# Performance work log

Measured on AMD Instinct MI355X. Metric: run time of the kernel, lower is better.

## Reference

```python
import jax, jax.numpy as jnp
import numpy as np

N_ROWS = 8192
EMBED_DIM = 256


def setup_inputs() -> dict:
    key = jax.random.key(0)
    k1, k2, k3, k4, k5 = jax.random.split(key, 5)
    M = jax.random.normal(k1, (N_ROWS, EMBED_DIM), dtype=jnp.float32)
    N = jax.random.normal(k2, (N_ROWS, EMBED_DIM), dtype=jnp.float32)
    # gate_w: nn.Linear(embed_dim, 1) -> weight [1, d], bias [1]; gate_b extra scalar param [1]
    Wg = jax.random.normal(k3, (1, EMBED_DIM), dtype=jnp.float32) * 0.06
    bg = jax.random.normal(k4, (1,), dtype=jnp.float32) * 0.1
    gate_b = jax.random.normal(k5, (1,), dtype=jnp.float32) * 0.1
    return {"M": M, "N": N, "Wg": Wg, "bg": bg, "gate_b": gate_b, "iseval": 0}


def reference(M, N, Wg, bg, gate_b, iseval):
    # mt: [n, n] cross-similarity scores
    mt = jnp.matmul(N, M.T)
    if not iseval:
        # training branch: zero out the diagonal (mt - diag(diag(mt)))
        n = mt.shape[0]
        idx = jnp.arange(n)
        mt = mt.at[idx, idx].set(0.0)
    else:
        # eval branch: zero out the first row
        mt = mt.at[0].set(0.0)
    attn_weight = jax.nn.softmax(mt, axis=-1)          # [n, n]
    out_attn = jnp.matmul(attn_weight, M)              # [n, d]
    gate = jax.nn.sigmoid(jnp.matmul(out_attn, Wg.T) + bg + gate_b)  # [n, 1]
    boosted = out_attn * gate + N * (1.0 - gate)       # [n, d]
    return boosted[:, None, None, :]                   # [n, 1, 1, d]
```

## Files before the change

### kernel.cpp

```cpp
#include <hip/hip_runtime.h>


constexpr int EMBED = 256;
constexpr int BQ = 64;
constexpr int BJ = 32;
constexpr int NT = 256;

constexpr int MH0  = 0;
constexpr int MH1  = 16384;
constexpr int MT0  = 32768;
constexpr int MT1  = 49152;
constexpr int SS_O = 65536;
constexpr int PH_O = 74752;
constexpr int MS_O = 79872;
constexpr int LS_O = 80128;
constexpr int AS_O = 80384;
constexpr int LDS_TOTAL = 80640;

typedef _Float16 half8 __attribute__((ext_vector_type(8)));
typedef float f32x4 __attribute__((ext_vector_type(4)));
typedef short short8v __attribute__((ext_vector_type(8)));

static __device__ __forceinline__ f32x4 mfma16(half8 a, half8 b, f32x4 c) {
    return __builtin_amdgcn_mfma_f32_16x16x32_f16(a, b, c, 0, 0, 0);
}
static __device__ __forceinline__ void gld_lds16(const void* g, void* l) {
    __builtin_amdgcn_global_load_lds((const __attribute__((address_space(1))) unsigned int*)g,
                                     (__attribute__((address_space(3))) unsigned int*)l, 16, 0, 0);
}
static __device__ __forceinline__ short f2h(float x) {
    return (short)__builtin_bit_cast(unsigned short, (_Float16)x);
}

__global__ void prep(const float* __restrict__ M,
                     short* __restrict__ MhG, short* __restrict__ MtG) {
    __shared__ float L[32 * 260];
    const int blk = blockIdx.x;
    const int t = threadIdx.x;
    {
        const float* src = M + (size_t)(blk * 32 + (t >> 3)) * EMBED + (t & 7) * 32;
        float* lr = L + (t >> 3) * 260 + (t & 7) * 32;
        #pragma unroll
        for (int i = 0; i < 8; ++i)
            *(float4*)(lr + 4 * i) = *(const float4*)(src + 4 * i);
    }
    __syncthreads();
    {
        const int j = t >> 3, key = j & 7;
        short* dst = MhG + (size_t)(blk * 32 + j) * 256;
        #pragma unroll
        for (int cc = 0; cc < 4; ++cc) {
            int c = (t & 7) * 4 + cc;
            short8v v;
            #pragma unroll
            for (int e = 0; e < 8; ++e) v[e] = f2h(L[j * 260 + c * 8 + e]);
            *(short8v*)(dst + (c ^ key) * 8) = v;
        }
    }
    {
        const int P = t >> 1, hv = t & 1;
        short* dst = MtG + (size_t)blk * 8192 + P * 64;
        #pragma unroll
        for (int pp = 0; pp < 4; ++pp) {
            int p = hv * 4 + pp;
            int c = p ^ (P & 7);
            int d = 2 * P + (c >> 2), jc = c & 3;
            short8v v;
            #pragma unroll
            for (int e = 0; e < 8; ++e) v[e] = f2h(L[(jc * 8 + e) * 260 + d]);
            *(short8v*)(dst + p * 8) = v;
        }
    }
}

__launch_bounds__(NT, 2)
__global__ void attn_split4(const short* __restrict__ MhG, const short* __restrict__ MtG,
                            const float* __restrict__ Ng, const int* __restrict__ iseval_p,
                            float* __restrict__ O0out, short* __restrict__ Ofp,
                            float* __restrict__ MLm, float* __restrict__ MLl, int n)
{
    __shared__ __align__(16) char smem[LDS_TOTAL];
    float* SS = (float*)(smem + SS_O);
    float* MS = (float*)(smem + MS_O);
    float* LS = (float*)(smem + LS_O);
    float* AS = (float*)(smem + AS_O);

    const int t = threadIdx.x, lane = t & 63, wave = t >> 6;
    const int quad = lane >> 4, mn = lane & 15;
    const int qb = blockIdx.x & 127, s = blockIdx.x >> 7;
    const int q0 = qb * BQ;
    const int jbase = s * (n >> 2);
    const int ntiles = (n >> 2) / BJ;
    const int iseval = *iseval_p;
    const int qp = wave >> 1;
    const int jt = wave & 1;
    const int dh = wave & 1;
    const int sq = t >> 2, sh = t & 3;

    if (t < BQ) { MS[t] = -1e30f; LS[t] = 0.f; }

    half8 Qf[2][8];
    #pragma unroll
    for (int qi = 0; qi < 2; ++qi) {
        const float* np = Ng + (size_t)(q0 + (2 * qp + qi) * 16 + mn) * EMBED;
        #pragma unroll
        for (int ks = 0; ks < 8; ++ks) {
            const float* p = np + ks * 32 + quad * 8;
            float4 a = *(const float4*)p, b = *(const float4*)(p + 4);
            half8 h;
            h[0]=(_Float16)a.x; h[1]=(_Float16)a.y; h[2]=(_Float16)a.z; h[3]=(_Float16)a.w;
            h[4]=(_Float16)b.x; h[5]=(_Float16)b.y; h[6]=(_Float16)b.z; h[7]=(_Float16)b.w;
            Qf[qi][ks] = h;
        }
    }

    {
        const char* mh = (const char*)MhG + (size_t)jbase * 512;
        const char* mt = (const char*)MtG + (size_t)jbase * 512;
        #pragma unroll
        for (int i = 0; i < 4; ++i) {
            int cb = wave * 4 + i;
            gld_lds16(mh + cb * 1024 + lane * 16, smem + MH0 + cb * 1024);
            gld_lds16(mt + cb * 1024 + lane * 16, smem + MT0 + cb * 1024);
        }
    }

    f32x4 O[2][8];
    #pragma unroll
    for (int qi = 0; qi < 2; ++qi)
        #pragma unroll
        for (int dt = 0; dt < 8; ++dt) O[qi][dt] = (f32x4){0.f, 0.f, 0.f, 0.f};

    __syncthreads();

    const int brow = jt * 16 + mn;
    const int bkey = brow & 7;

    for (int tile = 0; tile < ntiles; ++tile) {
        const int cur = tile & 1;
        const char* mhc = smem + (cur ? MH1 : MH0);
        char*       mhn = smem + (cur ? MH0 : MH1);
        const char* mtc = smem + (cur ? MT1 : MT0);
        char*       mtn = smem + (cur ? MT0 : MT1);
        const int j0g = jbase + tile * BJ;
        const bool hn = (tile + 1) < ntiles;

        if (hn) {
            const char* mh = (const char*)MhG + (size_t)(j0g + BJ) * 512;
            #pragma unroll
            for (int i = 0; i < 4; ++i) {
                int cb = wave * 4 + i;
                gld_lds16(mh + cb * 1024 + lane * 16, mhn + cb * 1024);
            }
        }

        {
            f32x4 a0 = (f32x4){0.f,0.f,0.f,0.f}, a1 = (f32x4){0.f,0.f,0.f,0.f};
            #pragma unroll
            for (int ks = 0; ks < 8; ++ks) {
                half8 bf = *(const half8*)(mhc + brow * 512 + (((4 * ks + quad) ^ bkey) << 4));
                a0 = mfma16(Qf[0][ks], bf, a0);
                a1 = mfma16(Qf[1][ks], bf, a1);
            }
            #pragma unroll
            for (int r = 0; r < 4; ++r) {
                SS[((2 * qp) * 16 + quad * 4 + r) * 36 + jt * 16 + mn]     = a0[r];
                SS[((2 * qp + 1) * 16 + quad * 4 + r) * 36 + jt * 16 + mn] = a1[r];
            }
        }
        __syncthreads();

        if (hn) {
            const char* mt = (const char*)MtG + (size_t)(j0g + BJ) * 512;
            #pragma unroll
            for (int i = 0; i < 4; ++i) {
                int cb = wave * 4 + i;
                gld_lds16(mt + cb * 1024 + lane * 16, mtn + cb * 1024);
            }
        }

        {
            float4 sa = *(const float4*)(SS + sq * 36 + 8 * sh);
            float4 sb = *(const float4*)(SS + sq * 36 + 8 * sh + 4);
            float sv[8] = {sa.x, sa.y, sa.z, sa.w, sb.x, sb.y, sb.z, sb.w};
            const int qg = q0 + sq;
            if (iseval) {
                if (qg == 0) {
                    #pragma unroll
                    for (int i = 0; i < 8; ++i) sv[i] = 0.f;
                }
            } else {
                int dj = qg - j0g - 8 * sh;
                #pragma unroll
                for (int i = 0; i < 8; ++i) if (dj == i) sv[i] = 0.f;
            }
            float mx = sv[0];
            #pragma unroll
            for (int i = 1; i < 8; ++i) mx = fmaxf(mx, sv[i]);
            mx = fmaxf(mx, __shfl_xor(mx, 1));
            mx = fmaxf(mx, __shfl_xor(mx, 2));
            float m_old = MS[sq];
            float m_new = fmaxf(m_old, mx);
            float alpha = __expf(m_old - m_new);
            float p[8], ps = 0.f;
            #pragma unroll
            for (int i = 0; i < 8; ++i) { p[i] = __expf(sv[i] - m_new); ps += p[i]; }
            ps += __shfl_xor(ps, 1);
            ps += __shfl_xor(ps, 2);
            if (sh == 0) {
                MS[sq] = m_new;
                AS[sq] = alpha;
                LS[sq] = LS[sq] * alpha + ps;
            }
            half8 ph;
            #pragma unroll
            for (int i = 0; i < 8; ++i) ph[i] = (_Float16)p[i];
            *(half8*)(smem + PH_O + sq * 80 + sh * 16) = ph;
        }
        __syncthreads();

        {
            float aq[2][4];
            #pragma unroll
            for (int qi = 0; qi < 2; ++qi)
                #pragma unroll
                for (int r = 0; r < 4; ++r)
                    aq[qi][r] = AS[(2 * qp + qi) * 16 + quad * 4 + r];
            half8 pa[2];
            #pragma unroll
            for (int qi = 0; qi < 2; ++qi)
                pa[qi] = *(const half8*)(smem + PH_O + ((2 * qp + qi) * 16 + mn) * 80 + quad * 16);
            #pragma unroll
            for (int dt = 0; dt < 8; ++dt) {
                int d = dh * 128 + dt * 16 + mn;
                int P2 = d >> 1;
                int p = ((d & 1) * 4 + quad) ^ (P2 & 7);
                half8 bf = *(const half8*)(mtc + P2 * 128 + p * 16);
                #pragma unroll
                for (int qi = 0; qi < 2; ++qi) {
                    f32x4 o = O[qi][dt];
                    o[0] *= aq[qi][0]; o[1] *= aq[qi][1]; o[2] *= aq[qi][2]; o[3] *= aq[qi][3];
                    O[qi][dt] = mfma16(pa[qi], bf, o);
                }
            }
        }
    }

    if (s == 0) {
        #pragma unroll
        for (int qi = 0; qi < 2; ++qi) {
            int qtb = q0 + (2 * qp + qi) * 16;
            #pragma unroll
            for (int dt = 0; dt < 8; ++dt) {
                int col = dh * 128 + dt * 16 + mn;
                #pragma unroll
                for (int r = 0; r < 4; ++r)
                    O0out[(size_t)(qtb + quad * 4 + r) * EMBED + col] = O[qi][dt][r];
            }
        }
    } else {
        short* dst = Ofp + (size_t)(s - 1) * n * EMBED;
        #pragma unroll
        for (int qi = 0; qi < 2; ++qi) {
            int qtb = q0 + (2 * qp + qi) * 16;
            #pragma unroll
            for (int dt = 0; dt < 8; ++dt) {
                int col = dh * 128 + dt * 16 + mn;
                #pragma unroll
                for (int r = 0; r < 4; ++r)
                    dst[(size_t)(qtb + quad * 4 + r) * EMBED + col] = f2h(O[qi][dt][r]);
            }
        }
    }
    if (t < BQ) {
        MLm[s * n + q0 + t] = MS[t];
        MLl[s * n + q0 + t] = LS[t];
    }
}

__global__ void combine4(const float* __restrict__ O0, const short* __restrict__ Ofp,
                         const float* __restrict__ MLm, const float* __restrict__ MLl,
                         const float* __restrict__ Ng, const float* __restrict__ Wg,
                         const float* __restrict__ bg, const float* __restrict__ gb,
                         float* __restrict__ out, int n)
{
    const int t = threadIdx.x;
    const int row = blockIdx.x * 16 + (t >> 4);
    const int c = t & 15;
    float ms[4], ls[4];
    #pragma unroll
    for (int s = 0; s < 4; ++s) { ms[s] = MLm[s * n + row]; ls[s] = MLl[s * n + row]; }
    float m = fmaxf(fmaxf(ms[0], ms[1]), fmaxf(ms[2], ms[3]));
    float w[4], lsum = 0.f;
    #pragma unroll
    for (int s = 0; s < 4; ++s) { w[s] = __expf(ms[s] - m); lsum += w[s] * ls[s]; }
    float linv = 1.f / lsum;

    float acc[16];
    {
        const float4* o0 = (const float4*)(O0 + (size_t)row * EMBED + c * 16);
        #pragma unroll
        for (int i = 0; i < 4; ++i) {
            float4 v = o0[i];
            acc[4*i+0] = w[0] * v.x; acc[4*i+1] = w[0] * v.y;
            acc[4*i+2] = w[0] * v.z; acc[4*i+3] = w[0] * v.w;
        }
    }
    #pragma unroll
    for (int s = 1; s < 4; ++s) {
        const short* op = Ofp + (size_t)(s - 1) * n * EMBED + (size_t)row * EMBED + c * 16;
        half8 a = *(const half8*)op, b = *(const half8*)(op + 8);
        #pragma unroll
        for (int i = 0; i < 8; ++i) {
            acc[i]     += w[s] * (float)a[i];
            acc[8 + i] += w[s] * (float)b[i];
        }
    }
    float dot = 0.f;
    #pragma unroll
    for (int i = 0; i < 16; ++i) { acc[i] *= linv; dot += acc[i] * Wg[c * 16 + i]; }
    dot += __shfl_xor(dot, 1);
    dot += __shfl_xor(dot, 2);
    dot += __shfl_xor(dot, 4);
    dot += __shfl_xor(dot, 8);
    float g = 1.f / (1.f + __expf(-(dot + bg[0] + gb[0])));
    const float4* n4 = (const float4*)(Ng + (size_t)row * EMBED + c * 16);
    float4* o4 = (float4*)(out + (size_t)row * EMBED + c * 16);
    #pragma unroll
    for (int i = 0; i < 4; ++i) {
        float4 nn = n4[i];
        float4 res;
        res.x = acc[4*i+0] * g + nn.x * (1.f - g);
        res.y = acc[4*i+1] * g + nn.y * (1.f - g);
        res.z = acc[4*i+2] * g + nn.z * (1.f - g);
        res.w = acc[4*i+3] * g + nn.w * (1.f - g);
        o4[i] = res;
    }
}

extern "C" void kernel_launch(void* const* d_in, const int* in_sizes, int n_in,
                              void* d_out, int out_size, void* d_ws, size_t ws_size,
                              hipStream_t stream) {
    const float* M      = (const float*)d_in[0];
    const float* N      = (const float*)d_in[1];
    const float* Wgp    = (const float*)d_in[2];
    const float* bgp    = (const float*)d_in[3];
    const float* gbp    = (const float*)d_in[4];
    const int*   iseval = (const int*)d_in[5];
    float* out = (float*)d_out;

    int n = in_sizes[0] / EMBED;
    short* MhG = (short*)d_ws;
    short* MtG = MhG + (size_t)n * EMBED;
    short* Ofp = MtG + (size_t)n * EMBED;
    float* MLm = (float*)(Ofp + (size_t)3 * n * EMBED);
    float* MLl = MLm + 4 * n;

    hipLaunchKernelGGL(prep, dim3(n / 32), dim3(256), 0, stream, M, MhG, MtG);
    hipLaunchKernelGGL(attn_split4, dim3((n / BQ) * 4), dim3(NT), 0, stream,
                       MhG, MtG, N, iseval, out, Ofp, MLm, MLl, n);
    hipLaunchKernelGGL(combine4, dim3(n / 16), dim3(256), 0, stream,
                       out, Ofp, MLm, MLl, N, Wgp, bgp, gbp, out, n);
}
```

Baseline: 217.7 us.

## Load K/V fragments straight from global into registers, split QK by K-halves

```diff
diff --git a/kernel.cpp b/kernel.cpp
--- a/kernel.cpp
+++ b/kernel.cpp
@@ -6,16 +6,12 @@
 constexpr int BJ = 32;
 constexpr int NT = 256;
 
-constexpr int MH0  = 0;
-constexpr int MH1  = 16384;
-constexpr int MT0  = 32768;
-constexpr int MT1  = 49152;
-constexpr int SS_O = 65536;
-constexpr int PH_O = 74752;
-constexpr int MS_O = 79872;
-constexpr int LS_O = 80128;
-constexpr int AS_O = 80384;
-constexpr int LDS_TOTAL = 80640;
+constexpr int SS_OFF = 0;
+constexpr int PH_OFF = 18432;
+constexpr int MS_OFF = 23552;
+constexpr int LS_OFF = 23808;
+constexpr int AS_OFF = 24064;
+constexpr int LDS_SZ = 24320;
 
 typedef _Float16 half8 __attribute__((ext_vector_type(8)));
 typedef float f32x4 __attribute__((ext_vector_type(4)));
@@ -24,165 +20,149 @@
 static __device__ __forceinline__ f32x4 mfma16(half8 a, half8 b, f32x4 c) {
     return __builtin_amdgcn_mfma_f32_16x16x32_f16(a, b, c, 0, 0, 0);
 }
-static __device__ __forceinline__ void gld_lds16(const void* g, void* l) {
-    __builtin_amdgcn_global_load_lds((const __attribute__((address_space(1))) unsigned int*)g,
-                                     (__attribute__((address_space(3))) unsigned int*)l, 16, 0, 0);
-}
 static __device__ __forceinline__ short f2h(float x) {
     return (short)__builtin_bit_cast(unsigned short, (_Float16)x);
 }
 
 __global__ void prep(const float* __restrict__ M,
                      short* __restrict__ MhG, short* __restrict__ MtG) {
-    __shared__ float L[32 * 260];
-    const int blk = blockIdx.x;
+    __shared__ float L[16 * 260];
+    const int r0 = blockIdx.x * 16;
     const int t = threadIdx.x;
+    const int pj = t >> 4, pc = (t & 15) * 16;
     {
-        const float* src = M + (size_t)(blk * 32 + (t >> 3)) * EMBED + (t & 7) * 32;
-        float* lr = L + (t >> 3) * 260 + (t & 7) * 32;
-        #pragma unroll
-        for (int i = 0; i < 8; ++i)
-            *(float4*)(lr + 4 * i) = *(const float4*)(src + 4 * i);
+        const float* src = M + (size_t)(r0 + pj) * EMBED + pc;
+        float4 v[4];
+        #pragma unroll
+        for (int i = 0; i < 4; ++i) v[i] = ((const float4*)src)[i];
+        short* hd = MhG + (size_t)(r0 + pj) * EMBED + pc;
+        #pragma unroll
+        for (int i = 0; i < 2; ++i) {
+            float4 a = v[2 * i], b = v[2 * i + 1];
+            short8v h;
+            h[0]=f2h(a.x); h[1]=f2h(a.y); h[2]=f2h(a.z); h[3]=f2h(a.w);
+            h[4]=f2h(b.x); h[5]=f2h(b.y); h[6]=f2h(b.z); h[7]=f2h(b.w);
+            *(short8v*)(hd + 8 * i) = h;
+        }
+        #pragma unroll
+        for (int i = 0; i < 4; ++i)
+            *(float4*)(L + pj * 260 + pc + 4 * i) = v[i];
     }
     __syncthreads();
     {
-        const int j = t >> 3, key = j & 7;
-        short* dst = MhG + (size_t)(blk * 32 + j) * 256;
-        #pragma unroll
-        for (int cc = 0; cc < 4; ++cc) {
-            int c = (t & 7) * 4 + cc;
-            short8v v;
-            #pragma unroll
-            for (int e = 0; e < 8; ++e) v[e] = f2h(L[j * 260 + c * 8 + e]);
-            *(short8v*)(dst + (c ^ key) * 8) = v;
-        }
-    }
-    {
-        const int P = t >> 1, hv = t & 1;
-        short* dst = MtG + (size_t)blk * 8192 + P * 64;
-        #pragma unroll
-        for (int pp = 0; pp < 4; ++pp) {
-            int p = hv * 4 + pp;
-            int c = p ^ (P & 7);
-            int d = 2 * P + (c >> 2), jc = c & 3;
-            short8v v;
-            #pragma unroll
-            for (int e = 0; e < 8; ++e) v[e] = f2h(L[(jc * 8 + e) * 260 + d]);
-            *(short8v*)(dst + p * 8) = v;
+        const int d = t;
+        const int tile = r0 >> 5, jh = (r0 >> 4) & 1;
+        short* dst = MtG + (size_t)tile * (BJ * EMBED) + d * BJ + jh * 16;
+        #pragma unroll
+        for (int g2 = 0; g2 < 2; ++g2) {
+            short8v w;
+            #pragma unroll
+            for (int e = 0; e < 8; ++e) w[e] = f2h(L[(g2 * 8 + e) * 260 + d]);
+            *(short8v*)(dst + g2 * 8) = w;
         }
     }
 }
 
 __launch_bounds__(NT, 2)
-__global__ void attn_split4(const short* __restrict__ MhG, const short* __restrict__ MtG,
-                            const float* __restrict__ Ng, const int* __restrict__ iseval_p,
-                            float* __restrict__ O0out, short* __restrict__ Ofp,
-                            float* __restrict__ MLm, float* __restrict__ MLl, int n)
+__global__ void attn(const short* __restrict__ MhG, const short* __restrict__ MtG,
+                     const float* __restrict__ Ng, const int* __restrict__ iseval_p,
+                     float* __restrict__ O0out, short* __restrict__ Ofp,
+                     float* __restrict__ MLm, float* __restrict__ MLl, int n)
 {
-    __shared__ __align__(16) char smem[LDS_TOTAL];
-    float* SS = (float*)(smem + SS_O);
-    float* MS = (float*)(smem + MS_O);
-    float* LS = (float*)(smem + LS_O);
-    float* AS = (float*)(smem + AS_O);
+    __shared__ __align__(16) char smem[LDS_SZ];
+    float* MS = (float*)(smem + MS_OFF);
+    float* LS = (float*)(smem + LS_OFF);
+    float* AS = (float*)(smem + AS_OFF);
 
     const int t = threadIdx.x, lane = t & 63, wave = t >> 6;
     const int quad = lane >> 4, mn = lane & 15;
-    const int qb = blockIdx.x & 127, s = blockIdx.x >> 7;
+    const int bid = blockIdx.x;
+    const int s  = (bid & 7) >> 1;
+    const int qb = ((bid >> 3) << 1) | (bid & 1);
     const int q0 = qb * BQ;
     const int jbase = s * (n >> 2);
+    const int jb32 = jbase / BJ;
     const int ntiles = (n >> 2) / BJ;
     const int iseval = *iseval_p;
-    const int qp = wave >> 1;
-    const int jt = wave & 1;
-    const int dh = wave & 1;
+    const int jt = wave & 1, kh = wave >> 1;
+    const int dq = wave;
     const int sq = t >> 2, sh = t & 3;
 
     if (t < BQ) { MS[t] = -1e30f; LS[t] = 0.f; }
 
-    half8 Qf[2][8];
-    #pragma unroll
-    for (int qi = 0; qi < 2; ++qi) {
-        const float* np = Ng + (size_t)(q0 + (2 * qp + qi) * 16 + mn) * EMBED;
-        #pragma unroll
-        for (int ks = 0; ks < 8; ++ks) {
-            const float* p = np + ks * 32 + quad * 8;
+    half8 Qf[4][4];
+    #pragma unroll
+    for (int qi = 0; qi < 4; ++qi) {
+        const float* np = Ng + (size_t)(q0 + qi * 16 + mn) * EMBED;
+        #pragma unroll
+        for (int kk = 0; kk < 4; ++kk) {
+            const float* p = np + (kh * 4 + kk) * 32 + quad * 8;
             float4 a = *(const float4*)p, b = *(const float4*)(p + 4);
             half8 h;
             h[0]=(_Float16)a.x; h[1]=(_Float16)a.y; h[2]=(_Float16)a.z; h[3]=(_Float16)a.w;
             h[4]=(_Float16)b.x; h[5]=(_Float16)b.y; h[6]=(_Float16)b.z; h[7]=(_Float16)b.w;
-            Qf[qi][ks] = h;
-        }
-    }
-
-    {
-        const char* mh = (const char*)MhG + (size_t)jbase * 512;
-        const char* mt = (const char*)MtG + (size_t)jbase * 512;
-        #pragma unroll
-        for (int i = 0; i < 4; ++i) {
-            int cb = wave * 4 + i;
-            gld_lds16(mh + cb * 1024 + lane * 16, smem + MH0 + cb * 1024);
-            gld_lds16(mt + cb * 1024 + lane * 16, smem + MT0 + cb * 1024);
-        }
-    }
-
-    f32x4 O[2][8];
-    #pragma unroll
-    for (int qi = 0; qi < 2; ++qi)
-        #pragma unroll
-        for (int dt = 0; dt < 8; ++dt) O[qi][dt] = (f32x4){0.f, 0.f, 0.f, 0.f};
+            Qf[qi][kk] = h;
+        }
+    }
+
+    f32x4 O[4][4];
+    #pragma unroll
+    for (int qi = 0; qi < 4; ++qi)
+        #pragma unroll
+        for (int dt = 0; dt < 4; ++dt) O[qi][dt] = (f32x4){0.f, 0.f, 0.f, 0.f};
+
+    const short* mhb0 = MhG + (size_t)(jbase + jt * 16 + mn) * EMBED + kh * 128 + quad * 8;
+    half8 Bc[4], Bn[4], Mtf[4];
+    #pragma unroll
+    for (int kk = 0; kk < 4; ++kk) Bc[kk] = *(const half8*)(mhb0 + kk * 32);
 
     __syncthreads();
 
-    const int brow = jt * 16 + mn;
-    const int bkey = brow & 7;
-
     for (int tile = 0; tile < ntiles; ++tile) {
-        const int cur = tile & 1;
-        const char* mhc = smem + (cur ? MH1 : MH0);
-        char*       mhn = smem + (cur ? MH0 : MH1);
-        const char* mtc = smem + (cur ? MT1 : MT0);
-        char*       mtn = smem + (cur ? MT0 : MT1);
         const int j0g = jbase + tile * BJ;
-        const bool hn = (tile + 1) < ntiles;
-
-        if (hn) {
-            const char* mh = (const char*)MhG + (size_t)(j0g + BJ) * 512;
-            #pragma unroll
-            for (int i = 0; i < 4; ++i) {
-                int cb = wave * 4 + i;
-                gld_lds16(mh + cb * 1024 + lane * 16, mhn + cb * 1024);
-            }
-        }
 
         {
-            f32x4 a0 = (f32x4){0.f,0.f,0.f,0.f}, a1 = (f32x4){0.f,0.f,0.f,0.f};
-            #pragma unroll
-            for (int ks = 0; ks < 8; ++ks) {
-                half8 bf = *(const half8*)(mhc + brow * 512 + (((4 * ks + quad) ^ bkey) << 4));
-                a0 = mfma16(Qf[0][ks], bf, a0);
-                a1 = mfma16(Qf[1][ks], bf, a1);
-            }
+            f32x4 a0 = (f32x4){0,0,0,0}, a1 = (f32x4){0,0,0,0};
+            f32x4 a2 = (f32x4){0,0,0,0}, a3 = (f32x4){0,0,0,0};
+            #pragma unroll
+            for (int kk = 0; kk < 4; ++kk) {
+                half8 bf = Bc[kk];
+                a0 = mfma16(Qf[0][kk], bf, a0);
+                a1 = mfma16(Qf[1][kk], bf, a1);
+                a2 = mfma16(Qf[2][kk], bf, a2);
+                a3 = mfma16(Qf[3][kk], bf, a3);
+            }
+            float* ssp = (float*)(smem + SS_OFF) + kh * 2304;
             #pragma unroll
             for (int r = 0; r < 4; ++r) {
-                SS[((2 * qp) * 16 + quad * 4 + r) * 36 + jt * 16 + mn]     = a0[r];
-                SS[((2 * qp + 1) * 16 + quad * 4 + r) * 36 + jt * 16 + mn] = a1[r];
+                ssp[(0  + quad * 4 + r) * 36 + jt * 16 + mn] = a0[r];
+                ssp[(16 + quad * 4 + r) * 36 + jt * 16 + mn] = a1[r];
+                ssp[(32 + quad * 4 + r) * 36 + jt * 16 + mn] = a2[r];
+                ssp[(48 + quad * 4 + r) * 36 + jt * 16 + mn] = a3[r];
             }
         }
         __syncthreads();
 
-        if (hn) {
-            const char* mt = (const char*)MtG + (size_t)(j0g + BJ) * 512;
-            #pragma unroll
-            for (int i = 0; i < 4; ++i) {
-                int cb = wave * 4 + i;
-                gld_lds16(mt + cb * 1024 + lane * 16, mtn + cb * 1024);
-            }
-        }
-
+        if (tile + 1 < ntiles) {
+            const short* nb = mhb0 + (size_t)(tile + 1) * (BJ * EMBED);
+            #pragma unroll
+            for (int kk = 0; kk < 4; ++kk) Bn[kk] = *(const half8*)(nb + kk * 32);
+        }
         {
-            float4 sa = *(const float4*)(SS + sq * 36 + 8 * sh);
-            float4 sb = *(const float4*)(SS + sq * 36 + 8 * sh + 4);
-            float sv[8] = {sa.x, sa.y, sa.z, sa.w, sb.x, sb.y, sb.z, sb.w};
+            const short* mtb = MtG + (size_t)(jb32 + tile) * (BJ * EMBED);
+            #pragma unroll
+            for (int dt = 0; dt < 4; ++dt)
+                Mtf[dt] = *(const half8*)(mtb + (dq * 64 + dt * 16 + mn) * BJ + quad * 8);
+        }
+
+        {
+            const float* p0 = (const float*)(smem + SS_OFF) + sq * 36 + 8 * sh;
+            float4 sa = *(const float4*)p0;
+            float4 sb = *(const float4*)(p0 + 4);
+            float4 sc = *(const float4*)(p0 + 2304);
+            float4 sd = *(const float4*)(p0 + 2308);
+            float sv[8] = {sa.x + sc.x, sa.y + sc.y, sa.z + sc.z, sa.w + sc.w,
+                           sb.x + sd.x, sb.y + sd.y, sb.z + sd.z, sb.w + sd.w};
             const int qg = q0 + sq;
             if (iseval) {
                 if (qg == 0) {
@@ -215,62 +195,46 @@
             half8 ph;
             #pragma unroll
             for (int i = 0; i < 8; ++i) ph[i] = (_Float16)p[i];
-            *(half8*)(smem + PH_O + sq * 80 + sh * 16) = ph;
+            *(half8*)(smem + PH_OFF + sq * 80 + sh * 16) = ph;
         }
         __syncthreads();
 
-        {
-            float aq[2][4];
-            #pragma unroll
-            for (int qi = 0; qi < 2; ++qi)
+        #pragma unroll
+        for (int qi = 0; qi < 4; ++qi) {
+            half8 pf = *(const half8*)(smem + PH_OFF + (qi * 16 + mn) * 80 + quad * 16);
+            f32x4 al = *(const f32x4*)((const float*)(smem + AS_OFF) + qi * 16 + quad * 4);
+            #pragma unroll
+            for (int dt = 0; dt < 4; ++dt) {
+                f32x4 o = O[qi][dt];
+                o[0] *= al[0]; o[1] *= al[1]; o[2] *= al[2]; o[3] *= al[3];
+                O[qi][dt] = mfma16(pf, Mtf[dt], o);
+            }
+        }
+        #pragma unroll
+        for (int kk = 0; kk < 4; ++kk) Bc[kk] = Bn[kk];
+    }
+
+    if (s == 0) {
+        #pragma unroll
+        for (int qi = 0; qi < 4; ++qi)
+            #pragma unroll
+            for (int dt = 0; dt < 4; ++dt) {
+                int col = dq * 64 + dt * 16 + mn;
                 #pragma unroll
                 for (int r = 0; r < 4; ++r)
-                    aq[qi][r] = AS[(2 * qp + qi) * 16 + quad * 4 + r];
-            half8 pa[2];
-            #pragma unroll
-            for (int qi = 0; qi < 2; ++qi)
-                pa[qi] = *(const half8*)(smem + PH_O + ((2 * qp + qi) * 16 + mn) * 80 + quad * 16);
-            #pragma unroll
-            for (int dt = 0; dt < 8; ++dt) {
-                int d = dh * 128 + dt * 16 + mn;
-                int P2 = d >> 1;
-                int p = ((d & 1) * 4 + quad) ^ (P2 & 7);
-                half8 bf = *(const half8*)(mtc + P2 * 128 + p * 16);
-                #pragma unroll
-                for (int qi = 0; qi < 2; ++qi) {
-                    f32x4 o = O[qi][dt];
-                    o[0] *= aq[qi][0]; o[1] *= aq[qi][1]; o[2] *= aq[qi][2]; o[3] *= aq[qi][3];
-                    O[qi][dt] = mfma16(pa[qi], bf, o);
-                }
-            }
-        }
-    }
-
-    if (s == 0) {
-        #pragma unroll
-        for (int qi = 0; qi < 2; ++qi) {
-            int qtb = q0 + (2 * qp + qi) * 16;
-            #pragma unroll
-            for (int dt = 0; dt < 8; ++dt) {
-                int col = dh * 128 + dt * 16 + mn;
+                    O0out[(size_t)(q0 + qi * 16 + quad * 4 + r) * EMBED + col] = O[qi][dt][r];
+            }
+    } else {
+        short* dst = Ofp + (size_t)(s - 1) * n * EMBED;
+        #pragma unroll
+        for (int qi = 0; qi < 4; ++qi)
+            #pragma unroll
+            for (int dt = 0; dt < 4; ++dt) {
+                int col = dq * 64 + dt * 16 + mn;
                 #pragma unroll
                 for (int r = 0; r < 4; ++r)
-                    O0out[(size_t)(qtb + quad * 4 + r) * EMBED + col] = O[qi][dt][r];
-            }
-        }
-    } else {
-        short* dst = Ofp + (size_t)(s - 1) * n * EMBED;
-        #pragma unroll
-        for (int qi = 0; qi < 2; ++qi) {
-            int qtb = q0 + (2 * qp + qi) * 16;
-            #pragma unroll
-            for (int dt = 0; dt < 8; ++dt) {
-                int col = dh * 128 + dt * 16 + mn;
-                #pragma unroll
-                for (int r = 0; r < 4; ++r)
-                    dst[(size_t)(qtb + quad * 4 + r) * EMBED + col] = f2h(O[qi][dt][r]);
-            }
-        }
+                    dst[(size_t)(q0 + qi * 16 + quad * 4 + r) * EMBED + col] = f2h(O[qi][dt][r]);
+            }
     }
     if (t < BQ) {
         MLm[s * n + q0 + t] = MS[t];
@@ -289,11 +253,11 @@
     const int c = t & 15;
     float ms[4], ls[4];
     #pragma unroll
-    for (int s = 0; s < 4; ++s) { ms[s] = MLm[s * n + row]; ls[s] = MLl[s * n + row]; }
+    for (int k = 0; k < 4; ++k) { ms[k] = MLm[k * n + row]; ls[k] = MLl[k * n + row]; }
     float m = fmaxf(fmaxf(ms[0], ms[1]), fmaxf(ms[2], ms[3]));
     float w[4], lsum = 0.f;
     #pragma unroll
-    for (int s = 0; s < 4; ++s) { w[s] = __expf(ms[s] - m); lsum += w[s] * ls[s]; }
+    for (int k = 0; k < 4; ++k) { w[k] = __expf(ms[k] - m); lsum += w[k] * ls[k]; }
     float linv = 1.f / lsum;
 
     float acc[16];
@@ -307,13 +271,13 @@
         }
     }
     #pragma unroll
-    for (int s = 1; s < 4; ++s) {
-        const short* op = Ofp + (size_t)(s - 1) * n * EMBED + (size_t)row * EMBED + c * 16;
+    for (int k = 1; k < 4; ++k) {
+        const short* op = Ofp + (size_t)(k - 1) * n * EMBED + (size_t)row * EMBED + c * 16;
         half8 a = *(const half8*)op, b = *(const half8*)(op + 8);
         #pragma unroll
         for (int i = 0; i < 8; ++i) {
-            acc[i]     += w[s] * (float)a[i];
-            acc[8 + i] += w[s] * (float)b[i];
+            acc[i]     += w[k] * (float)a[i];
+            acc[8 + i] += w[k] * (float)b[i];
         }
     }
     float dot = 0.f;
@@ -356,9 +320,9 @@
     float* MLm = (float*)(Ofp + (size_t)3 * n * EMBED);
     float* MLl = MLm + 4 * n;
 
-    hipLaunchKernelGGL(prep, dim3(n / 32), dim3(256), 0, stream, M, MhG, MtG);
-    hipLaunchKernelGGL(attn_split4, dim3((n / BQ) * 4), dim3(NT), 0, stream,
+    hipLaunchKernelGGL(prep, dim3(n / 16), dim3(NT), 0, stream, M, MhG, MtG);
+    hipLaunchKernelGGL(attn, dim3((n / BQ) * 4), dim3(NT), 0, stream,
                        MhG, MtG, N, iseval, out, Ofp, MLm, MLl, n);
-    hipLaunchKernelGGL(combine4, dim3(n / 16), dim3(256), 0, stream,
+    hipLaunchKernelGGL(combine4, dim3(n / 16), dim3(NT), 0, stream,
                        out, Ofp, MLm, MLl, N, Wgp, bgp, gbp, out, n);
 }
```

New measurement: 186.9 us. 1.16x faster.
